# Kernel tuning notes

Measured on AMD Instinct MI355X. Metric: run time of the kernel, lower is better.

Reference implementation:

```python
import jax, jax.numpy as jnp
import numpy as np

N_NODES = 50000
N_EDGES = 800000
N_FEAT = 128
HIDDEN = 128
HEADS = 4
C = HIDDEN // HEADS  # per-head channels = 32
N_LAYERS = 3
OUT_DIM = 2048
N_GRAPHS = 1000
LEAKY = 0.2  # PyG GATConv default negative_slope


def setup_inputs() -> dict:
    key = jax.random.key(0)
    ks = jax.random.split(key, 12)
    x = jax.random.normal(ks[0], (N_NODES, N_FEAT), dtype=jnp.float32)
    edge_index = jax.random.randint(ks[1], (2, N_EDGES), 0, N_NODES, dtype=jnp.int32)
    edge_attr = jax.random.normal(ks[2], (N_EDGES, 1), dtype=jnp.float32)
    batch = (jnp.arange(N_NODES, dtype=jnp.int32) // (N_NODES // N_GRAPHS))  # 50 nodes per graph
    s = 1.0 / np.sqrt(HIDDEN)
    Ws = jax.random.normal(ks[3], (N_LAYERS, N_FEAT, HIDDEN), dtype=jnp.float32) * s
    att_src = jax.random.normal(ks[4], (N_LAYERS, HEADS, C), dtype=jnp.float32) * s
    att_dst = jax.random.normal(ks[5], (N_LAYERS, HEADS, C), dtype=jnp.float32) * s
    We = jax.random.normal(ks[6], (N_LAYERS, 1, HIDDEN), dtype=jnp.float32) * s
    att_e = jax.random.normal(ks[7], (N_LAYERS, HEADS, C), dtype=jnp.float32) * s
    biases = jnp.zeros((N_LAYERS, HIDDEN), dtype=jnp.float32)
    lin1_w = jax.random.normal(ks[8], (HIDDEN, OUT_DIM), dtype=jnp.float32) * s
    lin1_b = jnp.zeros((OUT_DIM,), dtype=jnp.float32)
    return {"x": x, "edge_index": edge_index, "edge_attr": edge_attr, "batch": batch,
            "Ws": Ws, "att_src": att_src, "att_dst": att_dst, "We": We,
            "att_e": att_e, "biases": biases, "lin1_w": lin1_w, "lin1_b": lin1_b}


def _gat_layer(x, src, dst, ea, W, a_s, a_d, We_l, a_e, b):
    """PyG GATConv: shared lin for src/dst, edge_dim=1, concat heads, eval mode."""
    N = x.shape[0]
    h = (x @ W).reshape(N, HEADS, C)                       # [N,H,C]
    al_s = jnp.einsum('nhc,hc->nh', h, a_s)                # [N,H]
    al_d = jnp.einsum('nhc,hc->nh', h, a_d)
    e = (ea @ We_l).reshape(-1, HEADS, C)                  # [E',H,C]
    al_e = jnp.einsum('ehc,hc->eh', e, a_e)
    logits = jax.nn.leaky_relu(al_s[src] + al_d[dst] + al_e, LEAKY)  # [E',H]
    # segment softmax over incoming edges of each dst node, per head
    m = jax.ops.segment_max(logits, dst, num_segments=N)
    m = jnp.where(jnp.isfinite(m), m, 0.0)
    ex = jnp.exp(logits - m[dst])
    den = jax.ops.segment_sum(ex, dst, num_segments=N)
    alpha = ex / (den[dst] + 1e-16)                        # [E',H]
    msg = alpha[:, :, None] * h[src]                       # [E',H,C]
    out = jax.ops.segment_sum(msg, dst, num_segments=N)    # [N,H,C]
    return out.reshape(N, HIDDEN) + b


def reference(x, edge_index, edge_attr, batch, Ws, att_src, att_dst, We, att_e, biases, lin1_w, lin1_b):
    N = x.shape[0]
    src, dst = edge_index[0], edge_index[1]
    # add_self_loops=True with fill_value='mean' (PyG default): self-loop
    # edge_attr at node i = mean of edge_attr over edges pointing to i.
    cnt = jax.ops.segment_sum(jnp.ones_like(edge_attr[:, 0]), dst, num_segments=N)
    ea_sum = jax.ops.segment_sum(edge_attr, dst, num_segments=N)
    ea_self = jnp.where(cnt[:, None] > 0, ea_sum / jnp.maximum(cnt[:, None], 1.0), 0.0)
    loop = jnp.arange(N, dtype=src.dtype)
    src_f = jnp.concatenate([src, loop])
    dst_f = jnp.concatenate([dst, loop])
    ea_f = jnp.concatenate([edge_attr, ea_self], axis=0)
    for l in range(N_LAYERS):
        x = _gat_layer(x, src_f, dst_f, ea_f, Ws[l], att_src[l], att_dst[l], We[l], att_e[l], biases[l])
        x = jax.nn.relu(x)  # dropout is identity in eval mode
    pooled = jax.ops.segment_max(x, batch, num_segments=N_GRAPHS, indices_are_sorted=True)
    out = pooled @ lin1_w + lin1_b
    return jax.nn.sigmoid(out)  # classes_is_bit=True
```

## Files before the change

### kernel.cpp

```cpp
#include <hip/hip_runtime.h>
#include <hip/hip_bf16.h>
#include <math.h>

#define NN 50000
#define NE 800000
#define HID 128
#define HEADS 4
#define CH 32
#define NG 1000
#define OUTD 2048
#define LEAKY 0.2f
#define NB196 ((NN + 255) / 256)

typedef __attribute__((ext_vector_type(8))) short bshort8;
typedef __attribute__((ext_vector_type(4))) float floatx4;

__device__ __forceinline__ float lrelu(float v) { return fmaxf(v, LEAKY * v); }

__device__ __forceinline__ unsigned short f2bf(float f) {
    __hip_bfloat16 b = __float2bfloat16(f);
    return *reinterpret_cast<unsigned short*>(&b);
}
__device__ __forceinline__ float bflo(unsigned u) { return __uint_as_float(u << 16); }
__device__ __forceinline__ float bfhi(unsigned u) { return __uint_as_float(u & 0xffff0000u); }
__device__ __forceinline__ float bfu(unsigned short u) { return __uint_as_float(((unsigned)u) << 16); }

__global__ void k_hist(const int* __restrict__ ei, int* __restrict__ deg,
                       int* __restrict__ pos) {
    int e = blockIdx.x * 256 + threadIdx.x;
    if (e >= NE) return;
    pos[e] = atomicAdd(&deg[ei[NE + e]], 1);
}

__global__ __launch_bounds__(256) void k_s1(const int* __restrict__ deg,
                                            int* __restrict__ loc,
                                            int* __restrict__ bsum) {
    __shared__ int ws[4];
    int t = blockIdx.x * 256 + threadIdx.x;
    int lane = threadIdx.x & 63, wid = threadIdx.x >> 6;
    int v = (t < NN) ? deg[t] : 0;
    int run = v;
    for (int off = 1; off < 64; off <<= 1) {
        int u = __shfl_up(run, off);
        if (lane >= off) run += u;
    }
    if (lane == 63) ws[wid] = run;
    __syncthreads();
    int wadd = 0;
    if (wid > 0) wadd += ws[0];
    if (wid > 1) wadd += ws[1];
    if (wid > 2) wadd += ws[2];
    if (t < NN) loc[t] = run - v + wadd;
    if (threadIdx.x == 255) bsum[blockIdx.x] = wadd + run;
}

__global__ __launch_bounds__(256) void k_s2(const int* __restrict__ bsum,
                                            int* __restrict__ bexcl) {
    __shared__ int ws[4];
    int t = threadIdx.x;
    int lane = t & 63, wid = t >> 6;
    int v = (t < NB196) ? bsum[t] : 0;
    int run = v;
    for (int off = 1; off < 64; off <<= 1) {
        int u = __shfl_up(run, off);
        if (lane >= off) run += u;
    }
    if (lane == 63) ws[wid] = run;
    __syncthreads();
    int wadd = 0;
    if (wid > 0) wadd += ws[0];
    if (wid > 1) wadd += ws[1];
    if (wid > 2) wadd += ws[2];
    if (t < NB196) bexcl[t] = run - v + wadd;
}

__global__ __launch_bounds__(256) void k_s3(const int* __restrict__ loc,
                                            const int* __restrict__ bexcl,
                                            int* __restrict__ rowptr) {
    int t = blockIdx.x * 256 + threadIdx.x;
    if (t < NN) rowptr[t] = loc[t] + bexcl[blockIdx.x];
    if (t == 0) rowptr[NN] = NE;
}

__global__ void k_scatter(const int* __restrict__ ei, const float* __restrict__ ea,
                          const int* __restrict__ rowptr, const int* __restrict__ pos,
                          unsigned* __restrict__ ep) {
    int e = blockIdx.x * 256 + threadIdx.x;
    if (e >= NE) return;
    int d = ei[NE + e];
    unsigned rec = (((unsigned)f2bf(ea[e])) << 16) | (unsigned)ei[e];
    ep[rowptr[d] + pos[e]] = rec;
}

__global__ void k_coef(const float* __restrict__ We, const float* __restrict__ att_e,
                       float* __restrict__ coef) {
    int t = threadIdx.x;
    if (t < 12) {
        int l = t >> 2, hh = t & 3;
        const float* w = We + l * HID + hh * CH;
        const float* a = att_e + l * HID + hh * CH;
        float s = 0.f;
        for (int c = 0; c < CH; ++c) s += w[c] * a[c];
        coef[t] = s;
    }
}

__global__ void k_xcvt(const float* __restrict__ X, unsigned short* __restrict__ Xb) {
    int t = blockIdx.x * 256 + threadIdx.x;
    if (t >= NN * HID / 4) return;
    float4 v = ((const float4*)X)[t];
    ushort4 o;
    o.x = f2bf(v.x); o.y = f2bf(v.y); o.z = f2bf(v.z); o.w = f2bf(v.w);
    ((ushort4*)Xb)[t] = o;
}

__global__ void k_wt(const float* __restrict__ Ws, unsigned short* __restrict__ Wt) {
    int t = blockIdx.x * 256 + threadIdx.x;
    if (t >= 3 * HID * HID) return;
    int l = t / (HID * HID), rem = t % (HID * HID);
    int k = rem >> 7, n = rem & 127;
    Wt[l * HID * HID + n * HID + k] = f2bf(Ws[l * HID * HID + k * HID + n]);
}

__global__ __launch_bounds__(256) void k_mm(const unsigned short* __restrict__ Xb,
                                            const unsigned short* __restrict__ Wt,
                                            const float* __restrict__ aw_s,
                                            const float* __restrict__ aw_d,
                                            unsigned short* __restrict__ H2,
                                            float* __restrict__ als,
                                            float* __restrict__ ald) {
    int t = threadIdx.x;
    int wv = t >> 6, lane = t & 63;
    int m0 = blockIdx.x * 64 + wv * 16;
    int ln = lane & 15, kg = lane >> 4;
    int row = m0 + ln;
    int rc = row < NN ? row : NN - 1;
    floatx4 acc[8];
    #pragma unroll
    for (int nt = 0; nt < 8; ++nt) acc[nt] = (floatx4){0.f, 0.f, 0.f, 0.f};
    #pragma unroll
    for (int kc = 0; kc < HID; kc += 32) {
        bshort8 a = *(const bshort8*)&Xb[rc * HID + kc + kg * 8];
        #pragma unroll
        for (int nt = 0; nt < 8; ++nt) {
            bshort8 b = *(const bshort8*)&Wt[(nt * 16 + ln) * HID + kc + kg * 8];
            acc[nt] = __builtin_amdgcn_mfma_f32_16x16x32_bf16(a, b, acc[nt], 0, 0, 0);
        }
    }
    #pragma unroll
    for (int nt = 0; nt < 8; ++nt) {
        #pragma unroll
        for (int r = 0; r < 4; ++r) {
            int ro = m0 + kg * 4 + r;
            if (ro < NN) H2[ro * HID + nt * 16 + ln] = f2bf(acc[nt][r]);
        }
    }
    float ws8[8], wd8[8];
    #pragma unroll
    for (int nt = 0; nt < 8; ++nt) {
        ws8[nt] = aw_s[nt * 16 + ln];
        wd8[nt] = aw_d[nt * 16 + ln];
    }
    float pas[4][4], pad[4][4];
    #pragma unroll
    for (int h = 0; h < 4; ++h) {
        #pragma unroll
        for (int r = 0; r < 4; ++r) {
            pas[h][r] = acc[2 * h][r] * ws8[2 * h] + acc[2 * h + 1][r] * ws8[2 * h + 1];
            pad[h][r] = acc[2 * h][r] * wd8[2 * h] + acc[2 * h + 1][r] * wd8[2 * h + 1];
        }
    }
    #pragma unroll
    for (int h = 0; h < 4; ++h) {
        #pragma unroll
        for (int r = 0; r < 4; ++r) {
            #pragma unroll
            for (int off = 1; off < 16; off <<= 1) {
                pas[h][r] += __shfl_xor(pas[h][r], off);
                pad[h][r] += __shfl_xor(pad[h][r], off);
            }
        }
    }
    if (ln < 4) {
        #pragma unroll
        for (int r = 0; r < 4; ++r) {
            int ro = m0 + kg * 4 + r;
            if (ro < NN) {
                float vs = ln == 0 ? pas[0][r] : ln == 1 ? pas[1][r]
                         : ln == 2 ? pas[2][r] : pas[3][r];
                float vd = ln == 0 ? pad[0][r] : ln == 1 ? pad[1][r]
                         : ln == 2 ? pad[2][r] : pad[3][r];
                als[ro * 4 + ln] = vs;
                ald[ro * 4 + ln] = vd;
            }
        }
    }
}

__global__ __launch_bounds__(256) void k_agg(const int* __restrict__ rowptr,
                                             const unsigned* __restrict__ ep,
                                             const float* __restrict__ als,
                                             const float* __restrict__ ald,
                                             const unsigned short* __restrict__ H2,
                                             const float* __restrict__ coef_l,
                                             const float* __restrict__ bias,
                                             unsigned short* __restrict__ xout) {
    int n = blockIdx.x * 4 + (threadIdx.x >> 6);
    int lane = threadIdx.x & 63;
    int hp1 = lane & 3;
    int lq  = lane >> 2;
    int hp2 = lane >> 4;
    int c = lane * 2;
    const unsigned* H2w = (const unsigned*)H2;
    float coef1 = coef_l[hp1];
    float ald1 = ald[n * 4 + hp1];
    float s = 0.f, acc0 = 0.f, acc1 = 0.f, ea4 = 0.f;
    int jb = rowptr[n], je = rowptr[n + 1];
    int j0 = jb;
    for (; j0 + 16 <= je; j0 += 16) {
        unsigned rec = ep[j0 + lq];
        int srcp = rec & 0xffffu;
        float a = __uint_as_float(rec & 0xffff0000u);
        float p = __expf(lrelu(als[srcp * 4 + hp1] + ald1 + a * coef1));
        ea4 += a;
        float ps = p;
        ps += __shfl_xor(ps, 4);  ps += __shfl_xor(ps, 8);
        ps += __shfl_xor(ps, 16); ps += __shfl_xor(ps, 32);
        s += __uint_as_float(__builtin_amdgcn_ds_bpermute(hp2 << 2, __float_as_int(ps)));
        int pint = __float_as_int(p);
        #pragma unroll
        for (int k = 0; k < 16; ++k) {
            int srck = __builtin_amdgcn_readlane(srcp, 4 * k);
            float pk = __uint_as_float(
                __builtin_amdgcn_ds_bpermute((hp2 << 2) + 16 * k, pint));
            unsigned v = H2w[srck * 64 + lane];
            acc0 += pk * bflo(v);
            acc1 += pk * bfhi(v);
        }
    }
    if (j0 < je) {
        int eidx = j0 + lq;
        bool val = eidx < je;
        unsigned rec = val ? ep[eidx] : 0u;
        int srcp = rec & 0xffffu;
        float a = val ? __uint_as_float(rec & 0xffff0000u) : 0.f;
        float p = val ? __expf(lrelu(als[srcp * 4 + hp1] + ald1 + a * coef1)) : 0.f;
        ea4 += a;
        float ps = p;
        ps += __shfl_xor(ps, 4);  ps += __shfl_xor(ps, 8);
        ps += __shfl_xor(ps, 16); ps += __shfl_xor(ps, 32);
        s += __uint_as_float(__builtin_amdgcn_ds_bpermute(hp2 << 2, __float_as_int(ps)));
        int pint = __float_as_int(p);
        int nb = je - j0;
        for (int k = 0; k < nb; ++k) {
            int srck = __builtin_amdgcn_readlane(srcp, 4 * k);
            float pk = __uint_as_float(
                __builtin_amdgcn_ds_bpermute((hp2 << 2) + 16 * k, pint));
            unsigned v = H2w[srck * 64 + lane];
            acc0 += pk * bflo(v);
            acc1 += pk * bfhi(v);
        }
    }
    float easum = ea4;
    easum += __shfl_xor(easum, 1);  easum += __shfl_xor(easum, 2);
    easum += __shfl_xor(easum, 4);  easum += __shfl_xor(easum, 8);
    easum += __shfl_xor(easum, 16); easum += __shfl_xor(easum, 32);
    int degn = je - jb;
    float eaself = (degn > 0) ? easum / (4.0f * (float)degn) : 0.f;
    float coef2 = coef_l[hp2];
    float ald2 = ald[n * 4 + hp2];
    float ps = __expf(lrelu(als[n * 4 + hp2] + ald2 + eaself * coef2));
    unsigned vs = H2w[n * 64 + lane];
    s += ps;
    acc0 += ps * bflo(vs);
    acc1 += ps * bfhi(vs);
    float inv = 1.0f / (s + 1e-16f);
    float o0 = fmaxf(acc0 * inv + bias[c], 0.f);
    float o1 = fmaxf(acc1 * inv + bias[c + 1], 0.f);
    ushort2 ov;
    ov.x = f2bf(o0);
    ov.y = f2bf(o1);
    *(ushort2*)&xout[n * HID + c] = ov;
}

__global__ void k_pool(const unsigned short* __restrict__ x, float* __restrict__ pooled) {
    int g = blockIdx.x;
    int c = threadIdx.x;
    float m = -INFINITY;
    const unsigned short* p = x + g * 50 * HID + c;
    for (int i = 0; i < 50; ++i) m = fmaxf(m, bfu(p[i * HID]));
    pooled[g * HID + c] = m;
}

__global__ __launch_bounds__(256) void k_out(const float* __restrict__ pooled,
                                             const float* __restrict__ W,
                                             const float* __restrict__ b,
                                             float* __restrict__ out) {
    __shared__ float sp[8][HID];
    int t = threadIdx.x;
    int o = blockIdx.x * 256 + t;
    int g0 = blockIdx.y * 8;
    for (int i = t; i < 8 * HID / 4; i += 256)
        ((float4*)sp)[i] = ((const float4*)(pooled + g0 * HID))[i];
    __syncthreads();
    float acc[8];
    #pragma unroll
    for (int g = 0; g < 8; ++g) acc[g] = 0.f;
    for (int k = 0; k < HID; ++k) {
        float wv = W[k * OUTD + o];
        #pragma unroll
        for (int g = 0; g < 8; ++g) acc[g] += sp[g][k] * wv;
    }
    float bb = b[o];
    #pragma unroll
    for (int g = 0; g < 8; ++g)
        out[(g0 + g) * OUTD + o] = 1.f / (1.f + expf(-(acc[g] + bb)));
}

extern "C" void kernel_launch(void* const* d_in, const int* in_sizes, int n_in,
                              void* d_out, int out_size, void* d_ws, size_t ws_size,
                              hipStream_t stream) {
    const float* x_in    = (const float*)d_in[0];
    const int*   ei      = (const int*)d_in[1];
    const float* ea      = (const float*)d_in[2];
    const float* Ws      = (const float*)d_in[4];
    const float* att_src = (const float*)d_in[5];
    const float* att_dst = (const float*)d_in[6];
    const float* We      = (const float*)d_in[7];
    const float* att_e   = (const float*)d_in[8];
    const float* biases  = (const float*)d_in[9];
    const float* lin1_w  = (const float*)d_in[10];
    const float* lin1_b  = (const float*)d_in[11];
    float* out = (float*)d_out;

    char* p = (char*)d_ws;
    int*   deg    = (int*)p;                 p += sizeof(int) * NN;
    int*   loc    = (int*)p;                 p += sizeof(int) * NN;
    int*   bsum   = (int*)p;                 p += sizeof(int) * 256;
    int*   bexcl  = (int*)p;                 p += sizeof(int) * 256;
    int*   rowptr = (int*)p;                 p += sizeof(int) * (NN + 1);
    p += sizeof(int) * 3;
    int*   pos    = (int*)p;                 p += sizeof(int) * NE;
    unsigned* ep  = (unsigned*)p;            p += sizeof(unsigned) * NE;
    unsigned short* H2  = (unsigned short*)p; p += sizeof(short) * (size_t)NN * HID;
    unsigned short* Xb0 = (unsigned short*)p; p += sizeof(short) * (size_t)NN * HID;
    unsigned short* xa  = (unsigned short*)p; p += sizeof(short) * (size_t)NN * HID;
    unsigned short* xb  = (unsigned short*)p; p += sizeof(short) * (size_t)NN * HID;
    unsigned short* Wt  = (unsigned short*)p; p += sizeof(short) * 3 * HID * HID;
    float* als    = (float*)p;               p += sizeof(float) * NN * HEADS;
    float* ald    = (float*)p;               p += sizeof(float) * NN * HEADS;
    float* pooled = (float*)p;               p += sizeof(float) * NG * HID;
    float* coef   = (float*)p;               p += sizeof(float) * 12;

    hipMemsetAsync(deg, 0, sizeof(int) * NN, stream);
    k_hist<<<(NE + 255) / 256, 256, 0, stream>>>(ei, deg, pos);
    k_s1<<<NB196, 256, 0, stream>>>(deg, loc, bsum);
    k_s2<<<1, 256, 0, stream>>>(bsum, bexcl);
    k_s3<<<NB196, 256, 0, stream>>>(loc, bexcl, rowptr);
    k_scatter<<<(NE + 255) / 256, 256, 0, stream>>>(ei, ea, rowptr, pos, ep);
    k_coef<<<1, 64, 0, stream>>>(We, att_e, coef);
    k_wt<<<(3 * HID * HID + 255) / 256, 256, 0, stream>>>(Ws, Wt);
    k_xcvt<<<(NN * HID / 4 + 255) / 256, 256, 0, stream>>>(x_in, Xb0);

    for (int l = 0; l < 3; ++l) {
        const unsigned short* xin = (l == 0) ? Xb0 : (l == 1 ? xa : xb);
        unsigned short* xout      = (l == 1) ? xb : xa;
        k_mm<<<(NN + 63) / 64, 256, 0, stream>>>(xin, Wt + l * HID * HID,
                                                 att_src + l * HEADS * CH,
                                                 att_dst + l * HEADS * CH,
                                                 H2, als, ald);
        k_agg<<<NN / 4, 256, 0, stream>>>(rowptr, ep, als, ald,
                                          H2, coef + l * 4, biases + l * HID, xout);
    }
    k_pool<<<NG, HID, 0, stream>>>(xa, pooled);
    dim3 og(OUTD / 256, NG / 8);
    k_out<<<og, 256, 0, stream>>>(pooled, lin1_w, lin1_b, out);
}
```

Measured before the change: 430.9 us.

## Restructure GAT aggregation: 4 edges per wave in parallel with 16B row loads

The aggregation kernel now splits each wavefront into four 16-lane slots, each processing a different edge, with each lane loading 8 bf16 channels (16 bytes) of the source row and handling two edges per iteration. Partial sums are combined across slots with shuffles at the end, and only slot 0 writes the output. This replaces the per-edge readlane/bpermute broadcast loop and its serial 16-edge chain with wider vector gathers and more independent memory requests in flight. In exchange it adds a cross-slot reduction and idles three quarters of the wave on the store, and the edge buffer is padded by 8 entries.

```diff
diff --git a/kernel.cpp b/kernel.cpp
--- a/kernel.cpp
+++ b/kernel.cpp
@@ -207,80 +207,82 @@
                                              unsigned short* __restrict__ xout) {
     int n = blockIdx.x * 4 + (threadIdx.x >> 6);
     int lane = threadIdx.x & 63;
-    int hp1 = lane & 3;
-    int lq  = lane >> 2;
-    int hp2 = lane >> 4;
-    int c = lane * 2;
-    const unsigned* H2w = (const unsigned*)H2;
-    float coef1 = coef_l[hp1];
-    float ald1 = ald[n * 4 + hp1];
-    float s = 0.f, acc0 = 0.f, acc1 = 0.f, ea4 = 0.f;
+    int slot = lane >> 4, lpos = lane & 15;
+    int hh = lpos >> 2;
+    int ch0 = lpos * 8;
+    const uint4* H2q = (const uint4*)H2;
+    float coefh = coef_l[hh];
+    float aldh = ald[n * 4 + hh];
+    float s = 0.f, ea = 0.f;
+    float acc[8];
+    #pragma unroll
+    for (int i = 0; i < 8; ++i) acc[i] = 0.f;
     int jb = rowptr[n], je = rowptr[n + 1];
-    int j0 = jb;
-    for (; j0 + 16 <= je; j0 += 16) {
-        unsigned rec = ep[j0 + lq];
-        int srcp = rec & 0xffffu;
-        float a = __uint_as_float(rec & 0xffff0000u);
-        float p = __expf(lrelu(als[srcp * 4 + hp1] + ald1 + a * coef1));
-        ea4 += a;
-        float ps = p;
-        ps += __shfl_xor(ps, 4);  ps += __shfl_xor(ps, 8);
-        ps += __shfl_xor(ps, 16); ps += __shfl_xor(ps, 32);
-        s += __uint_as_float(__builtin_amdgcn_ds_bpermute(hp2 << 2, __float_as_int(ps)));
-        int pint = __float_as_int(p);
-        #pragma unroll
-        for (int k = 0; k < 16; ++k) {
-            int srck = __builtin_amdgcn_readlane(srcp, 4 * k);
-            float pk = __uint_as_float(
-                __builtin_amdgcn_ds_bpermute((hp2 << 2) + 16 * k, pint));
-            unsigned v = H2w[srck * 64 + lane];
-            acc0 += pk * bflo(v);
-            acc1 += pk * bfhi(v);
-        }
-    }
-    if (j0 < je) {
-        int eidx = j0 + lq;
-        bool val = eidx < je;
-        unsigned rec = val ? ep[eidx] : 0u;
-        int srcp = rec & 0xffffu;
-        float a = val ? __uint_as_float(rec & 0xffff0000u) : 0.f;
-        float p = val ? __expf(lrelu(als[srcp * 4 + hp1] + ald1 + a * coef1)) : 0.f;
-        ea4 += a;
-        float ps = p;
-        ps += __shfl_xor(ps, 4);  ps += __shfl_xor(ps, 8);
-        ps += __shfl_xor(ps, 16); ps += __shfl_xor(ps, 32);
-        s += __uint_as_float(__builtin_amdgcn_ds_bpermute(hp2 << 2, __float_as_int(ps)));
-        int pint = __float_as_int(p);
-        int nb = je - j0;
-        for (int k = 0; k < nb; ++k) {
-            int srck = __builtin_amdgcn_readlane(srcp, 4 * k);
-            float pk = __uint_as_float(
-                __builtin_amdgcn_ds_bpermute((hp2 << 2) + 16 * k, pint));
-            unsigned v = H2w[srck * 64 + lane];
-            acc0 += pk * bflo(v);
-            acc1 += pk * bfhi(v);
-        }
-    }
-    float easum = ea4;
-    easum += __shfl_xor(easum, 1);  easum += __shfl_xor(easum, 2);
-    easum += __shfl_xor(easum, 4);  easum += __shfl_xor(easum, 8);
-    easum += __shfl_xor(easum, 16); easum += __shfl_xor(easum, 32);
+    for (int j = jb; j < je; j += 8) {
+        int eA = j + slot;
+        bool vA = eA < je;
+        unsigned recA = vA ? ep[eA] : 0u;
+        int srcA = vA ? (int)(recA & 0xffffu) : n;
+        float aA = bfhi(recA);
+        uint4 hA = H2q[srcA * 16 + lpos];
+        float pA = vA ? __expf(lrelu(als[srcA * 4 + hh] + aldh + aA * coefh)) : 0.f;
+        int eB = j + 4 + slot;
+        bool vB = eB < je;
+        unsigned recB = vB ? ep[eB] : 0u;
+        int srcB = vB ? (int)(recB & 0xffffu) : n;
+        float aB = bfhi(recB);
+        uint4 hB = H2q[srcB * 16 + lpos];
+        float pB = vB ? __expf(lrelu(als[srcB * 4 + hh] + aldh + aB * coefh)) : 0.f;
+        s += pA + pB;
+        ea += aA + aB;
+        acc[0] += pA * bflo(hA.x) + pB * bflo(hB.x);
+        acc[1] += pA * bfhi(hA.x) + pB * bfhi(hB.x);
+        acc[2] += pA * bflo(hA.y) + pB * bflo(hB.y);
+        acc[3] += pA * bfhi(hA.y) + pB * bfhi(hB.y);
+        acc[4] += pA * bflo(hA.z) + pB * bflo(hB.z);
+        acc[5] += pA * bfhi(hA.z) + pB * bfhi(hB.z);
+        acc[6] += pA * bflo(hA.w) + pB * bflo(hB.w);
+        acc[7] += pA * bfhi(hA.w) + pB * bfhi(hB.w);
+    }
+    #pragma unroll
+    for (int i = 0; i < 8; ++i) {
+        acc[i] += __shfl_xor(acc[i], 16);
+        acc[i] += __shfl_xor(acc[i], 32);
+    }
+    s += __shfl_xor(s, 16);  s += __shfl_xor(s, 32);
+    ea += __shfl_xor(ea, 16); ea += __shfl_xor(ea, 32);
     int degn = je - jb;
-    float eaself = (degn > 0) ? easum / (4.0f * (float)degn) : 0.f;
-    float coef2 = coef_l[hp2];
-    float ald2 = ald[n * 4 + hp2];
-    float ps = __expf(lrelu(als[n * 4 + hp2] + ald2 + eaself * coef2));
-    unsigned vs = H2w[n * 64 + lane];
+    float eaself = (degn > 0) ? ea / (float)degn : 0.f;
+    float ps = __expf(lrelu(als[n * 4 + hh] + aldh + eaself * coefh));
+    uint4 hv = H2q[n * 16 + lpos];
     s += ps;
-    acc0 += ps * bflo(vs);
-    acc1 += ps * bfhi(vs);
+    acc[0] += ps * bflo(hv.x);
+    acc[1] += ps * bfhi(hv.x);
+    acc[2] += ps * bflo(hv.y);
+    acc[3] += ps * bfhi(hv.y);
+    acc[4] += ps * bflo(hv.z);
+    acc[5] += ps * bfhi(hv.z);
+    acc[6] += ps * bflo(hv.w);
+    acc[7] += ps * bfhi(hv.w);
     float inv = 1.0f / (s + 1e-16f);
-    float o0 = fmaxf(acc0 * inv + bias[c], 0.f);
-    float o1 = fmaxf(acc1 * inv + bias[c + 1], 0.f);
-    ushort2 ov;
-    ov.x = f2bf(o0);
-    ov.y = f2bf(o1);
-    *(ushort2*)&xout[n * HID + c] = ov;
+    if (slot == 0) {
+        float4 b0 = *(const float4*)&bias[ch0];
+        float4 b1 = *(const float4*)&bias[ch0 + 4];
+        float o0 = fmaxf(acc[0] * inv + b0.x, 0.f);
+        float o1 = fmaxf(acc[1] * inv + b0.y, 0.f);
+        float o2 = fmaxf(acc[2] * inv + b0.z, 0.f);
+        float o3 = fmaxf(acc[3] * inv + b0.w, 0.f);
+        float o4 = fmaxf(acc[4] * inv + b1.x, 0.f);
+        float o5 = fmaxf(acc[5] * inv + b1.y, 0.f);
+        float o6 = fmaxf(acc[6] * inv + b1.z, 0.f);
+        float o7 = fmaxf(acc[7] * inv + b1.w, 0.f);
+        uint4 ov;
+        ov.x = (((unsigned)f2bf(o1)) << 16) | f2bf(o0);
+        ov.y = (((unsigned)f2bf(o3)) << 16) | f2bf(o2);
+        ov.z = (((unsigned)f2bf(o5)) << 16) | f2bf(o4);
+        ov.w = (((unsigned)f2bf(o7)) << 16) | f2bf(o6);
+        *(uint4*)&xout[n * HID + ch0] = ov;
+    }
 }
 
 __global__ void k_pool(const unsigned short* __restrict__ x, float* __restrict__ pooled) {
@@ -341,7 +343,7 @@
     int*   rowptr = (int*)p;                 p += sizeof(int) * (NN + 1);
     p += sizeof(int) * 3;
     int*   pos    = (int*)p;                 p += sizeof(int) * NE;
-    unsigned* ep  = (unsigned*)p;            p += sizeof(unsigned) * NE;
+    unsigned* ep  = (unsigned*)p;            p += sizeof(unsigned) * (NE + 8);
     unsigned short* H2  = (unsigned short*)p; p += sizeof(short) * (size_t)NN * HID;
     unsigned short* Xb0 = (unsigned short*)p; p += sizeof(short) * (size_t)NN * HID;
     unsigned short* xa  = (unsigned short*)p; p += sizeof(short) * (size_t)NN * HID;
```

After: 411.6 us. -4.5%, faster.
